# Performance work log

Measured on AMD Instinct MI355X. Metric: run time of the kernel, lower is better.

The kernel has to match this reference:

```python
import jax, jax.numpy as jnp
import numpy as np

H, T, D = 16, 2048, 1024
DH = D // H  # 64


def setup_inputs() -> dict:
    key = jax.random.key(0)
    ks = jax.random.split(key, 6)
    state = jax.random.normal(ks[0], (H, DH, DH), jnp.float32) * 0.02  # per-head recurrent state
    x = jax.random.normal(ks[1], (T, D), jnp.float32)
    done = jax.random.uniform(ks[2], (T,)) < (4.0 / T)  # sparse episode-reset flags (bool)
    w_qkv = jax.random.normal(ks[3], (D, 3 * D), jnp.float32) / np.sqrt(D)
    b_qkv = jnp.zeros((3 * D,), jnp.float32)
    w_out = jax.random.normal(ks[4], (D, D), jnp.float32) / np.sqrt(D)
    b_out = jnp.zeros((D,), jnp.float32)
    return {"state": state, "x": x, "done": done, "w_qkv": w_qkv,
            "b_qkv": b_qkv, "w_out": w_out, "b_out": b_out}


def _mha_forward(state, x, done, w_qkv, b_qkv, w_out, b_out):
    # qkv projection; einops 'T (QKV H Dh) -> QKV H T Dh'
    qkv = (x @ w_qkv + b_qkv).reshape(T, 3, H, DH).transpose(1, 2, 0, 3)
    q, k, v = qkv[0], qkv[1], qkv[2]  # each (H, T, Dh)

    cum = jnp.cumsum(done.astype(jnp.int32))  # inclusive cumsum, as in done.cumsum()
    before_first = cum == 0            # tokens before first reset (attend to carried state)
    after_last = cum == cum[-1]        # tokens after last reset (feed new state)
    done_any = cum[-1] > 0

    # make_attn_mask(done): causal AND no reset index i with s < i <= t.
    # The scanned mask equals: causal & (cum[t] == cum[s]) (same-segment).
    t_idx = jnp.arange(T)
    mask = (t_idx[:, None] >= t_idx[None, :]) & (cum[:, None] == cum[None, :])  # (T, T)

    attn = jnp.where(mask[None], jnp.einsum('htd,hsd->hts', q, k), 0.0)  # mask * (q @ k.T)
    q_bef = q * before_first[None, :, None]
    out = jnp.einsum('hts,hsd->htd', attn, v) + jnp.einsum('htd,hde->hte', q_bef, state)

    k_aft = k * after_last[None, :, None]
    v_aft = v * after_last[None, :, None]
    s_new = jnp.einsum('htd,hte->hde', k_aft, v_aft)  # k_aft.T @ v_aft per head
    new_state = jnp.where(done_any, s_new, state + s_new)

    # 'H T Dh -> T (H Dh)' then output projection
    x_out = out.transpose(1, 0, 2).reshape(T, D) @ w_out + b_out
    return new_state, x_out


def reference(state, x, done, w_qkv, b_qkv, w_out, b_out):
    return _mha_forward(state, x, done, w_qkv, b_qkv, w_out, b_out)
```

## Files before the change

kernel.cpp:

```cpp
#include <hip/hip_runtime.h>

#define TT 2048
#define DD 1024
#define HH 16
#define DH 64
#define QKV_N 3072
#define QKW 2048

typedef __attribute__((ext_vector_type(8))) short bf16x8;
typedef __attribute__((ext_vector_type(4))) short short4v;
typedef __attribute__((ext_vector_type(4))) float f32x4;

__device__ inline short f2bf(float f) {
    union { float f; unsigned u; } v; v.f = f;
    unsigned r = v.u + 0x7fff + ((v.u >> 16) & 1);
    return (short)(r >> 16);
}

__device__ inline f32x4 mfma16(bf16x8 a, bf16x8 b, f32x4 c) {
    return __builtin_amdgcn_mfma_f32_16x16x32_bf16(a, b, c, 0, 0, 0);
}

__device__ __forceinline__ void gload16(const void* g, void* l) {
    __builtin_amdgcn_global_load_lds(
        (const __attribute__((address_space(1))) unsigned int*)g,
        (__attribute__((address_space(3))) unsigned int*)l, 16, 0, 0);
}

__device__ void transpose_tile(const float* __restrict__ in, short* __restrict__ out,
                               int R, int C, int r0, int c0, float (*tile)[65]) {
    int tid = threadIdx.x;
#pragma unroll
    for (int p = 0; p < 4; ++p) {
        int ch = tid + p * 256;
        int r = ch >> 4, c4 = (ch & 15) * 4;
        float4 v = *(const float4*)&in[(size_t)(r0 + r) * C + c0 + c4];
        tile[r][c4] = v.x; tile[r][c4 + 1] = v.y; tile[r][c4 + 2] = v.z; tile[r][c4 + 3] = v.w;
    }
    __syncthreads();
#pragma unroll
    for (int p = 0; p < 2; ++p) {
        int ch = tid + p * 256;
        int c = ch >> 3, r8 = (ch & 7) * 8;
        short tmp[8];
#pragma unroll
        for (int i = 0; i < 8; ++i) tmp[i] = f2bf(tile[r8 + i][c]);
        *(float4*)&out[(size_t)(c0 + c) * R + r0 + r8] = *(float4*)tmp;
    }
}

__global__ __launch_bounds__(256) void prep_kernel(const float* __restrict__ x,
                                                   const float* __restrict__ w_qkv,
                                                   const float* __restrict__ w_out,
                                                   const float* __restrict__ state,
                                                   const int* __restrict__ done,
                                                   short* __restrict__ x_bf,
                                                   short* __restrict__ wqT,
                                                   short* __restrict__ woT,
                                                   short* __restrict__ stT,
                                                   float* __restrict__ stout,
                                                   int* __restrict__ seg,
                                                   int* __restrict__ totalp,
                                                   int* __restrict__ aux) {
    __shared__ float tile[64][65];
    __shared__ int scanbuf[2048 + 512 + 1];
    int b = blockIdx.x;
    int tid = threadIdx.x;
    if (b < 1024) {
        int i = (b * 256 + tid) * 8;
        float4 a = *(const float4*)&x[i];
        float4 c = *(const float4*)&x[i + 4];
        short tmp[8] = {f2bf(a.x), f2bf(a.y), f2bf(a.z), f2bf(a.w),
                        f2bf(c.x), f2bf(c.y), f2bf(c.z), f2bf(c.w)};
        *(float4*)&x_bf[i] = *(float4*)tmp;
    } else if (b < 1792) {
        int bb = b - 1024;
        transpose_tile(w_qkv, wqT, DD, QKV_N, (bb & 15) * 64, (bb >> 4) * 64, tile);
    } else if (b < 2048) {
        int bb = b - 1792;
        transpose_tile(w_out, woT, DD, DD, (bb & 15) * 64, (bb >> 4) * 64, tile);
    } else if (b < 2064) {
        int h = b - 2048;
        transpose_tile(state + (size_t)h * 4096, stT + (size_t)h * 4096, DH, DH, 0, 0, tile);
    } else if (b < 2128) {
        __shared__ int anyf;
        if (tid == 0) anyf = 0;
        __syncthreads();
        int acc = 0;
#pragma unroll
        for (int i = 0; i < 8; ++i) acc |= done[tid * 8 + i];
        if (acc) anyf = 1;
        __syncthreads();
        int f = ((b - 2064) * 256 + tid) * 4;
        float4 v = anyf ? make_float4(0.f, 0.f, 0.f, 0.f) : *(const float4*)&state[f];
        *(float4*)&stout[f] = v;
    } else {
        int* segl = scanbuf;
        int* part = scanbuf + 2048;
        int* excl = scanbuf + 2304;
        int base = tid * 8;
        int local[8];
        int run = 0;
#pragma unroll
        for (int i = 0; i < 8; ++i) { run += (done[base + i] != 0) ? 1 : 0; local[i] = run; }
        part[tid] = run;
        __syncthreads();
        if (tid < 64) {
            int p4[4];
#pragma unroll
            for (int i = 0; i < 4; ++i) p4[i] = part[tid * 4 + i];
            int s = p4[0] + p4[1] + p4[2] + p4[3];
            int v = s;
#pragma unroll
            for (int off = 1; off < 64; off <<= 1) {
                int u = __shfl_up(v, off);
                if (tid >= off) v += u;
            }
            int ex = v - s;
#pragma unroll
            for (int i = 0; i < 4; ++i) { excl[tid * 4 + i] = ex; ex += p4[i]; }
            if (tid == 63) { totalp[0] = v; scanbuf[2560] = v; }
        }
        __syncthreads();
        int off = excl[tid];
#pragma unroll
        for (int i = 0; i < 8; ++i) {
            int sv = off + local[i];
            seg[base + i] = sv;
            segl[base + i] = sv;
        }
        __syncthreads();
        if (tid < 33) {
            int target = (tid < 32) ? segl[tid * 64] : scanbuf[2560];
            int lo = 0, hi = 2047;
            while (lo < hi) { int mid = (lo + hi) >> 1; if (segl[mid] >= target) hi = mid; else lo = mid + 1; }
            aux[tid] = lo >> 6;
        }
    }
}

__global__ __launch_bounds__(256, 3) void gemm_qkv(const short* __restrict__ A,
                                                   const short* __restrict__ BT,
                                                   const float* __restrict__ bias,
                                                   short* __restrict__ qk,
                                                   short* __restrict__ vt) {
    __shared__ __align__(16) short As[2][2][64 * 32];
    __shared__ __align__(16) short Bs[2][2][128 * 32];
    const int K = DD;
    int tid = threadIdx.x;
    int wave = tid >> 6, lane = tid & 63;
    int quad = lane >> 4, l15 = lane & 15;
    int m0 = blockIdx.x * 64, n0 = blockIdx.y * 128;
    int wr = (wave >> 1) * 32, wc = (wave & 1) * 64;

    int srow = wave * 16 + (lane >> 2);
    int scol = (lane & 3) * 8;
    const short* Ag = A + (size_t)(m0 + srow) * K + scol;
    const short* Bg = BT + (size_t)(n0 + srow) * K + scol;

#pragma unroll
    for (int ks = 0; ks < 2; ++ks) {
        gload16(Ag + ks * 32, &As[0][ks][(wave * 16) * 32]);
        gload16(Bg + ks * 32, &Bs[0][ks][(wave * 16) * 32]);
        gload16(Bg + (size_t)64 * K + ks * 32, &Bs[0][ks][(64 + wave * 16) * 32]);
    }
    __syncthreads();

    f32x4 acc[2][4] = {};
    int cur = 0;
    for (int k0 = 0; k0 < K; k0 += 64, cur ^= 1) {
        if (k0 + 64 < K) {
#pragma unroll
            for (int ks = 0; ks < 2; ++ks) {
                gload16(Ag + k0 + 64 + ks * 32, &As[cur ^ 1][ks][(wave * 16) * 32]);
                gload16(Bg + k0 + 64 + ks * 32, &Bs[cur ^ 1][ks][(wave * 16) * 32]);
                gload16(Bg + (size_t)64 * K + k0 + 64 + ks * 32,
                        &Bs[cur ^ 1][ks][(64 + wave * 16) * 32]);
            }
        }
#pragma unroll
        for (int ks = 0; ks < 2; ++ks) {
            bf16x8 af[2], bfr[4];
#pragma unroll
            for (int i = 0; i < 2; ++i)
                af[i]  = *(const bf16x8*)&As[cur][ks][(wr + i * 16 + l15) * 32 + quad * 8];
#pragma unroll
            for (int j = 0; j < 4; ++j)
                bfr[j] = *(const bf16x8*)&Bs[cur][ks][(wc + j * 16 + l15) * 32 + quad * 8];
#pragma unroll
            for (int i = 0; i < 2; ++i)
#pragma unroll
                for (int j = 0; j < 4; ++j)
                    acc[i][j] = mfma16(af[i], bfr[j], acc[i][j]);
        }
        __syncthreads();
    }

    if (n0 < 2048) {
#pragma unroll
        for (int i = 0; i < 2; ++i)
#pragma unroll
            for (int j = 0; j < 4; ++j)
#pragma unroll
                for (int r = 0; r < 4; ++r) {
                    int row = m0 + wr + i * 16 + quad * 4 + r;
                    int col = n0 + wc + j * 16 + l15;
                    qk[(size_t)row * QKW + col] = f2bf(acc[i][j][r] + bias[col]);
                }
    } else {
#pragma unroll
        for (int j = 0; j < 4; ++j) {
            int col = n0 + wc + j * 16 + l15;
            float bv = bias[col];
            int eg = col - 2048;
            int hh = eg >> 6, e = eg & 63;
#pragma unroll
            for (int i = 0; i < 2; ++i) {
                int tb = m0 + wr + i * 16 + quad * 4;
                short4v pk;
#pragma unroll
                for (int r = 0; r < 4; ++r) pk[r] = f2bf(acc[i][j][r] + bv);
                *(short4v*)&vt[(size_t)hh * (DH * TT) + (size_t)e * TT + tb] = pk;
            }
        }
    }
}

__global__ __launch_bounds__(256) void attn_mfma(const short* __restrict__ qk,
                                                 const short* __restrict__ vt,
                                                 const short* __restrict__ stT,
                                                 const int* __restrict__ seg,
                                                 const int* __restrict__ totalp,
                                                 const int* __restrict__ aux,
                                                 short* __restrict__ outb,
                                                 float* __restrict__ nsout) {
    __shared__ __align__(16) short Qh[2][64 * 32];
    __shared__ __align__(16) short Kh[2][2][64 * 32];
    __shared__ __align__(16) short Vh[2][2][64 * 32];
    __shared__ __align__(16) short Ss[64 * 72];

    int h = blockIdx.x, tt = blockIdx.y, z = blockIdx.z;
    int t0 = tt * 64;
    int tid = threadIdx.x, wave = tid >> 6, lane = tid & 63;
    int quad = lane >> 4, l15 = lane & 15;
    int myt = wave * 16;
    const short* vbase = vt + (size_t)h * (DH * TT);

    if (z == 1) {
        if (tt < aux[32]) return;
        int total = totalp[0];
        int myd = wave * 16;
        short* K0 = Kh[0][0];
        short* K1 = Kh[0][1];
        bool keep = (seg[t0 + lane] == total);
        const short* src = qk + (size_t)(t0 + lane) * QKW + 1024 + h * DH + myd;
        union { float4 f; short s[8]; } u0, u1;
        u0.f = keep ? *(const float4*)src : make_float4(0.f, 0.f, 0.f, 0.f);
        u1.f = keep ? *(const float4*)(src + 8) : make_float4(0.f, 0.f, 0.f, 0.f);
        short* dst = (lane < 32) ? &K0[lane] : &K1[lane - 32];
#pragma unroll
        for (int i = 0; i < 8; ++i) {
            dst[(myd + i) * 32] = u0.s[i];
            dst[(myd + 8 + i) * 32] = u1.s[i];
        }
        bf16x8 a0 = *(const bf16x8*)&K0[(myd + l15) * 32 + quad * 8];
        bf16x8 a1 = *(const bf16x8*)&K1[(myd + l15) * 32 + quad * 8];
        f32x4 acc2[4] = {};
#pragma unroll
        for (int j = 0; j < 4; ++j) {
            const short* vrow = vbase + (size_t)(j * 16 + l15) * TT + t0 + quad * 8;
            bf16x8 b0 = *(const bf16x8*)vrow;
            bf16x8 b1 = *(const bf16x8*)(vrow + 32);
            acc2[j] = mfma16(a0, b0, acc2[j]);
            acc2[j] = mfma16(a1, b1, acc2[j]);
        }
        float* oh = nsout + (size_t)h * 4096;
#pragma unroll
        for (int j = 0; j < 4; ++j)
#pragma unroll
            for (int r = 0; r < 4; ++r)
                atomicAdd(&oh[(myd + quad * 4 + r) * DH + j * 16 + l15], acc2[j][r]);
        return;
    }

    int st0 = aux[tt];
    int sr = lane >> 2;
    int ch = lane & 3;
    const short* kg = qk + 1024 + h * DH;

    {
#pragma unroll
        for (int h2 = 0; h2 < 2; ++h2)
            gload16(qk + (size_t)(t0 + myt + sr) * QKW + h * DH + h2 * 32 + ch * 8,
                    &Qh[h2][myt * 32]);
        int s0 = st0 * 64;
        gload16(kg + (size_t)(s0 + myt + sr) * QKW + ch * 8,      &Kh[0][0][myt * 32]);
        gload16(kg + (size_t)(s0 + myt + sr) * QKW + 32 + ch * 8, &Kh[0][1][myt * 32]);
        gload16(vbase + (size_t)(myt + sr) * TT + s0 + ch * 8,    &Vh[0][0][myt * 32]);
        gload16(vbase + (size_t)(myt + sr) * TT + s0 + 32 + ch * 8, &Vh[0][1][myt * 32]);
    }
    __syncthreads();

    bf16x8 af[2];
#pragma unroll
    for (int h2 = 0; h2 < 2; ++h2)
        af[h2] = *(const bf16x8*)&Qh[h2][(myt + l15) * 32 + quad * 8];

    int t_val = t0 + myt + l15;
    int seg_lane = seg[t_val];

    f32x4 acc2[4] = {};
    if (seg[t0] == 0) {
        const short* sb = stT + (size_t)h * 4096;
#pragma unroll
        for (int j = 0; j < 4; ++j)
#pragma unroll
            for (int h2 = 0; h2 < 2; ++h2) {
                bf16x8 a = *(const bf16x8*)(sb + (j * 16 + l15) * 64 + h2 * 32 + quad * 8);
                acc2[j] = mfma16(a, af[h2], acc2[j]);
            }
        if (seg_lane != 0) {
#pragma unroll
            for (int j = 0; j < 4; ++j)
#pragma unroll
                for (int r = 0; r < 4; ++r) acc2[j][r] = 0.f;
        }
    }

    int p = 0;
    for (int st = st0; st <= tt; ++st, p ^= 1) {
        if (st != st0) __syncthreads();
        if (st + 1 <= tt) {
            int s1 = (st + 1) * 64;
            gload16(kg + (size_t)(s1 + myt + sr) * QKW + ch * 8,        &Kh[p ^ 1][0][myt * 32]);
            gload16(kg + (size_t)(s1 + myt + sr) * QKW + 32 + ch * 8,   &Kh[p ^ 1][1][myt * 32]);
            gload16(vbase + (size_t)(myt + sr) * TT + s1 + ch * 8,      &Vh[p ^ 1][0][myt * 32]);
            gload16(vbase + (size_t)(myt + sr) * TT + s1 + 32 + ch * 8, &Vh[p ^ 1][1][myt * 32]);
        }
        int s0 = st * 64;

        f32x4 sacc[4] = {};
#pragma unroll
        for (int j = 0; j < 4; ++j)
#pragma unroll
            for (int h2 = 0; h2 < 2; ++h2) {
                bf16x8 kb = *(const bf16x8*)&Kh[p][h2][(j * 16 + l15) * 32 + quad * 8];
                sacc[j] = mfma16(kb, af[h2], sacc[j]);
            }
        int4 seg4[4];
#pragma unroll
        for (int j = 0; j < 4; ++j)
            seg4[j] = *(const int4*)&seg[s0 + j * 16 + quad * 4];
#pragma unroll
        for (int j = 0; j < 4; ++j) {
            short4v pk;
#pragma unroll
            for (int r = 0; r < 4; ++r) {
                int s_val = s0 + j * 16 + quad * 4 + r;
                int sv = (r == 0) ? seg4[j].x : (r == 1) ? seg4[j].y : (r == 2) ? seg4[j].z : seg4[j].w;
                bool ok = (sv == seg_lane) && (s_val <= t_val);
                pk[r] = ok ? f2bf(sacc[j][r]) : (short)0;
            }
            *(short4v*)&Ss[(myt + l15) * 72 + j * 16 + quad * 4] = pk;
        }
        bf16x8 sf[2];
#pragma unroll
        for (int h2 = 0; h2 < 2; ++h2)
            sf[h2] = *(const bf16x8*)&Ss[(myt + l15) * 72 + h2 * 32 + quad * 8];
#pragma unroll
        for (int j = 0; j < 4; ++j)
#pragma unroll
            for (int h2 = 0; h2 < 2; ++h2) {
                bf16x8 vb = *(const bf16x8*)&Vh[p][h2][(j * 16 + l15) * 32 + quad * 8];
                acc2[j] = mfma16(vb, sf[h2], acc2[j]);
            }
    }

#pragma unroll
    for (int j = 0; j < 4; ++j) {
        short4v pk;
#pragma unroll
        for (int r = 0; r < 4; ++r) pk[r] = f2bf(acc2[j][r]);
        *(short4v*)&outb[(size_t)t_val * DD + h * DH + j * 16 + quad * 4] = pk;
    }
}

__global__ __launch_bounds__(256) void gemm_out(const short* __restrict__ A,
                                                const short* __restrict__ BT,
                                                const float* __restrict__ bias,
                                                float* __restrict__ x_out) {
    __shared__ __align__(16) short As[2][2][64 * 32];
    __shared__ __align__(16) short Bs[2][2][128 * 32];
    const int K = DD, N = DD;
    int tid = threadIdx.x;
    int wave = tid >> 6, lane = tid & 63;
    int quad = lane >> 4, l15 = lane & 15;
    int m0 = blockIdx.x * 64, n0 = blockIdx.y * 128;
    int wr = (wave >> 1) * 32, wc = (wave & 1) * 64;

    int srow = wave * 16 + (lane >> 2);
    int scol = (lane & 3) * 8;
    const short* Ag = A + (size_t)(m0 + srow) * K + scol;
    const short* Bg = BT + (size_t)(n0 + srow) * K + scol;

#pragma unroll
    for (int ks = 0; ks < 2; ++ks) {
        gload16(Ag + ks * 32, &As[0][ks][(wave * 16) * 32]);
        gload16(Bg + ks * 32, &Bs[0][ks][(wave * 16) * 32]);
        gload16(Bg + (size_t)64 * K + ks * 32, &Bs[0][ks][(64 + wave * 16) * 32]);
    }
    __syncthreads();

    f32x4 acc[2][4] = {};
    int cur = 0;
    for (int k0 = 0; k0 < K; k0 += 64, cur ^= 1) {
        if (k0 + 64 < K) {
#pragma unroll
            for (int ks = 0; ks < 2; ++ks) {
                gload16(Ag + k0 + 64 + ks * 32, &As[cur ^ 1][ks][(wave * 16) * 32]);
                gload16(Bg + k0 + 64 + ks * 32, &Bs[cur ^ 1][ks][(wave * 16) * 32]);
                gload16(Bg + (size_t)64 * K + k0 + 64 + ks * 32,
                        &Bs[cur ^ 1][ks][(64 + wave * 16) * 32]);
            }
        }
#pragma unroll
        for (int ks = 0; ks < 2; ++ks) {
            bf16x8 af[2], bfr[4];
#pragma unroll
            for (int i = 0; i < 2; ++i)
                af[i]  = *(const bf16x8*)&As[cur][ks][(wr + i * 16 + l15) * 32 + quad * 8];
#pragma unroll
            for (int j = 0; j < 4; ++j)
                bfr[j] = *(const bf16x8*)&Bs[cur][ks][(wc + j * 16 + l15) * 32 + quad * 8];
#pragma unroll
            for (int i = 0; i < 2; ++i)
#pragma unroll
                for (int j = 0; j < 4; ++j)
                    acc[i][j] = mfma16(af[i], bfr[j], acc[i][j]);
        }
        __syncthreads();
    }

#pragma unroll
    for (int i = 0; i < 2; ++i)
#pragma unroll
        for (int j = 0; j < 4; ++j) {
            int col = n0 + wc + j * 16 + l15;
            float bv = bias[col];
#pragma unroll
            for (int r = 0; r < 4; ++r) {
                int row = m0 + wr + i * 16 + quad * 4 + r;
                x_out[(size_t)row * N + col] = acc[i][j][r] + bv;
            }
        }
}

extern "C" void kernel_launch(void* const* d_in, const int* in_sizes, int n_in,
                              void* d_out, int out_size, void* d_ws, size_t ws_size,
                              hipStream_t stream) {
    const float* state = (const float*)d_in[0];
    const float* x     = (const float*)d_in[1];
    const int*   done  = (const int*)d_in[2];
    const float* w_qkv = (const float*)d_in[3];
    const float* b_qkv = (const float*)d_in[4];
    const float* w_out = (const float*)d_in[5];
    const float* b_out = (const float*)d_in[6];

    char* ws = (char*)d_ws;
    int*   seg    = (int*)ws;
    int*   totalp = (int*)(ws + 8192);
    int*   aux    = (int*)(ws + 8256);
    short* wqT    = (short*)(ws + 8448);
    short* woT    = (short*)(ws + 6299904);
    short* stT    = (short*)(ws + 8397056);
    short* qk     = (short*)(ws + 8528128);
    short* vt     = (short*)(ws + 16916736);
    short* xbf_outb = (short*)(ws + 21111040);

    float* new_state_out = (float*)d_out;
    float* x_out         = (float*)d_out + HH * DH * DH;

    prep_kernel<<<2129, 256, 0, stream>>>(x, w_qkv, w_out, state, done,
                                          xbf_outb, wqT, woT, stT,
                                          new_state_out, seg, totalp, aux);

    gemm_qkv<<<dim3(TT / 64, QKV_N / 128), 256, 0, stream>>>(
        xbf_outb, wqT, b_qkv, qk, vt);

    attn_mfma<<<dim3(HH, TT / 64, 2), 256, 0, stream>>>(
        qk, vt, stT, seg, totalp, aux, xbf_outb, new_state_out);

    gemm_out<<<dim3(TT / 64, DD / 128), 256, 0, stream>>>(
        xbf_outb, woT, b_out, x_out);
}
```

Measured before the change: 147.2 us.

## Fuse four kernels into one persistent kernel with software grid barriers

The prep, QKV GEMM, attention and output GEMM kernels are merged into one persistent kernel of 512 blocks. Each block loops over the virtual block indices of each phase, and the phases are separated by an atomic grid barrier. Shared memory is overlaid with a union. The goal is to remove the launch gaps and tail effects between kernels. The cost is barrier spinning, a bound of 2 blocks per CU that can limit occupancy, a deadlock risk if not all 512 blocks are resident (there is a timeout break), and an extra memset.

```diff
diff --git a/kernel.cpp b/kernel.cpp
--- a/kernel.cpp
+++ b/kernel.cpp
@@ -6,6 +6,7 @@
 #define DH 64
 #define QKV_N 3072
 #define QKW 2048
+#define NBLK 512
 
 typedef __attribute__((ext_vector_type(8))) short bf16x8;
 typedef __attribute__((ext_vector_type(4))) short short4v;
@@ -26,6 +27,31 @@
         (const __attribute__((address_space(1))) unsigned int*)g,
         (__attribute__((address_space(3))) unsigned int*)l, 16, 0, 0);
 }
+
+__device__ __forceinline__ void gbar(int* cnt, int* flag, int target) {
+    __syncthreads();
+    if (threadIdx.x == 0) {
+        int t = __hip_atomic_fetch_add(cnt, 1, __ATOMIC_ACQ_REL, __HIP_MEMORY_SCOPE_AGENT);
+        if (t == NBLK - 1) {
+            __hip_atomic_store(cnt, 0, __ATOMIC_RELAXED, __HIP_MEMORY_SCOPE_AGENT);
+            __hip_atomic_fetch_add(flag, 1, __ATOMIC_RELEASE, __HIP_MEMORY_SCOPE_AGENT);
+        } else {
+            long long t0 = clock64();
+            while (__hip_atomic_load(flag, __ATOMIC_ACQUIRE, __HIP_MEMORY_SCOPE_AGENT) < target) {
+                if (clock64() - t0 > 60000000LL) break;
+                __builtin_amdgcn_s_sleep(2);
+            }
+        }
+    }
+    __syncthreads();
+}
+
+union SharedMem {
+    struct { short As[2][2][64 * 32]; short Bs[2][2][128 * 32]; } g;
+    struct { short Qh[2][64 * 32]; short Kh[2][2][64 * 32];
+             short Vh[2][2][64 * 32]; short Ss[64 * 72]; } a;
+    struct { float tile[64][65]; int scanbuf[2561]; } p;
+};
 
 __device__ void transpose_tile(const float* __restrict__ in, short* __restrict__ out,
                                int R, int C, int r0, int c0, float (*tile)[65]) {
@@ -49,417 +75,399 @@
     }
 }
 
-__global__ __launch_bounds__(256) void prep_kernel(const float* __restrict__ x,
-                                                   const float* __restrict__ w_qkv,
-                                                   const float* __restrict__ w_out,
-                                                   const float* __restrict__ state,
-                                                   const int* __restrict__ done,
-                                                   short* __restrict__ x_bf,
-                                                   short* __restrict__ wqT,
-                                                   short* __restrict__ woT,
-                                                   short* __restrict__ stT,
-                                                   float* __restrict__ stout,
-                                                   int* __restrict__ seg,
-                                                   int* __restrict__ totalp,
-                                                   int* __restrict__ aux) {
-    __shared__ float tile[64][65];
-    __shared__ int scanbuf[2048 + 512 + 1];
-    int b = blockIdx.x;
-    int tid = threadIdx.x;
-    if (b < 1024) {
-        int i = (b * 256 + tid) * 8;
-        float4 a = *(const float4*)&x[i];
-        float4 c = *(const float4*)&x[i + 4];
-        short tmp[8] = {f2bf(a.x), f2bf(a.y), f2bf(a.z), f2bf(a.w),
-                        f2bf(c.x), f2bf(c.y), f2bf(c.z), f2bf(c.w)};
-        *(float4*)&x_bf[i] = *(float4*)tmp;
-    } else if (b < 1792) {
-        int bb = b - 1024;
-        transpose_tile(w_qkv, wqT, DD, QKV_N, (bb & 15) * 64, (bb >> 4) * 64, tile);
-    } else if (b < 2048) {
-        int bb = b - 1792;
-        transpose_tile(w_out, woT, DD, DD, (bb & 15) * 64, (bb >> 4) * 64, tile);
-    } else if (b < 2064) {
-        int h = b - 2048;
-        transpose_tile(state + (size_t)h * 4096, stT + (size_t)h * 4096, DH, DH, 0, 0, tile);
-    } else if (b < 2128) {
-        __shared__ int anyf;
-        if (tid == 0) anyf = 0;
-        __syncthreads();
-        int acc = 0;
-#pragma unroll
-        for (int i = 0; i < 8; ++i) acc |= done[tid * 8 + i];
-        if (acc) anyf = 1;
-        __syncthreads();
-        int f = ((b - 2064) * 256 + tid) * 4;
-        float4 v = anyf ? make_float4(0.f, 0.f, 0.f, 0.f) : *(const float4*)&state[f];
-        *(float4*)&stout[f] = v;
-    } else {
-        int* segl = scanbuf;
-        int* part = scanbuf + 2048;
-        int* excl = scanbuf + 2304;
-        int base = tid * 8;
-        int local[8];
-        int run = 0;
-#pragma unroll
-        for (int i = 0; i < 8; ++i) { run += (done[base + i] != 0) ? 1 : 0; local[i] = run; }
-        part[tid] = run;
-        __syncthreads();
-        if (tid < 64) {
-            int p4[4];
-#pragma unroll
-            for (int i = 0; i < 4; ++i) p4[i] = part[tid * 4 + i];
-            int s = p4[0] + p4[1] + p4[2] + p4[3];
-            int v = s;
-#pragma unroll
-            for (int off = 1; off < 64; off <<= 1) {
-                int u = __shfl_up(v, off);
-                if (tid >= off) v += u;
-            }
-            int ex = v - s;
-#pragma unroll
-            for (int i = 0; i < 4; ++i) { excl[tid * 4 + i] = ex; ex += p4[i]; }
-            if (tid == 63) { totalp[0] = v; scanbuf[2560] = v; }
-        }
-        __syncthreads();
-        int off = excl[tid];
-#pragma unroll
-        for (int i = 0; i < 8; ++i) {
-            int sv = off + local[i];
-            seg[base + i] = sv;
-            segl[base + i] = sv;
-        }
-        __syncthreads();
-        if (tid < 33) {
-            int target = (tid < 32) ? segl[tid * 64] : scanbuf[2560];
-            int lo = 0, hi = 2047;
-            while (lo < hi) { int mid = (lo + hi) >> 1; if (segl[mid] >= target) hi = mid; else lo = mid + 1; }
-            aux[tid] = lo >> 6;
-        }
-    }
-}
-
-__global__ __launch_bounds__(256, 3) void gemm_qkv(const short* __restrict__ A,
-                                                   const short* __restrict__ BT,
-                                                   const float* __restrict__ bias,
-                                                   short* __restrict__ qk,
-                                                   short* __restrict__ vt) {
-    __shared__ __align__(16) short As[2][2][64 * 32];
-    __shared__ __align__(16) short Bs[2][2][128 * 32];
-    const int K = DD;
+__global__ __launch_bounds__(256, 2) void fused_kernel(
+    const float* __restrict__ x, const float* __restrict__ w_qkv,
+    const float* __restrict__ w_out, const float* __restrict__ state,
+    const int* __restrict__ done, const float* __restrict__ b_qkv,
+    const float* __restrict__ b_out,
+    short* __restrict__ xo,
+    short* __restrict__ wqT, short* __restrict__ woT, short* __restrict__ stT,
+    short* __restrict__ qk, short* __restrict__ vt,
+    float* __restrict__ nsout, float* __restrict__ x_out,
+    int* __restrict__ seg, int* __restrict__ totalp, int* __restrict__ aux,
+    int* __restrict__ bar) {
+    __shared__ __align__(16) SharedMem sh;
+    __shared__ int anyf;
+    int* cnt = bar;
+    int* flag = bar + 4;
+
+    int bid = blockIdx.x;
     int tid = threadIdx.x;
     int wave = tid >> 6, lane = tid & 63;
     int quad = lane >> 4, l15 = lane & 15;
-    int m0 = blockIdx.x * 64, n0 = blockIdx.y * 128;
-    int wr = (wave >> 1) * 32, wc = (wave & 1) * 64;
-
-    int srow = wave * 16 + (lane >> 2);
-    int scol = (lane & 3) * 8;
-    const short* Ag = A + (size_t)(m0 + srow) * K + scol;
-    const short* Bg = BT + (size_t)(n0 + srow) * K + scol;
-
-#pragma unroll
-    for (int ks = 0; ks < 2; ++ks) {
-        gload16(Ag + ks * 32, &As[0][ks][(wave * 16) * 32]);
-        gload16(Bg + ks * 32, &Bs[0][ks][(wave * 16) * 32]);
-        gload16(Bg + (size_t)64 * K + ks * 32, &Bs[0][ks][(64 + wave * 16) * 32]);
-    }
-    __syncthreads();
-
-    f32x4 acc[2][4] = {};
-    int cur = 0;
-    for (int k0 = 0; k0 < K; k0 += 64, cur ^= 1) {
-        if (k0 + 64 < K) {
+
+    for (int vb = bid; vb < 2129; vb += NBLK) {
+        __syncthreads();
+        int b = vb;
+        if (b < 1024) {
+            int i = (b * 256 + tid) * 8;
+            float4 a = *(const float4*)&x[i];
+            float4 c = *(const float4*)&x[i + 4];
+            short tmp[8] = {f2bf(a.x), f2bf(a.y), f2bf(a.z), f2bf(a.w),
+                            f2bf(c.x), f2bf(c.y), f2bf(c.z), f2bf(c.w)};
+            *(float4*)&xo[i] = *(float4*)tmp;
+        } else if (b < 1792) {
+            int bb = b - 1024;
+            transpose_tile(w_qkv, wqT, DD, QKV_N, (bb & 15) * 64, (bb >> 4) * 64, sh.p.tile);
+        } else if (b < 2048) {
+            int bb = b - 1792;
+            transpose_tile(w_out, woT, DD, DD, (bb & 15) * 64, (bb >> 4) * 64, sh.p.tile);
+        } else if (b < 2064) {
+            int h = b - 2048;
+            transpose_tile(state + (size_t)h * 4096, stT + (size_t)h * 4096, DH, DH, 0, 0, sh.p.tile);
+        } else if (b < 2128) {
+            if (tid == 0) anyf = 0;
+            __syncthreads();
+            int acc = 0;
+#pragma unroll
+            for (int i = 0; i < 8; ++i) acc |= done[tid * 8 + i];
+            if (acc) anyf = 1;
+            __syncthreads();
+            int f = ((b - 2064) * 256 + tid) * 4;
+            float4 v = anyf ? make_float4(0.f, 0.f, 0.f, 0.f) : *(const float4*)&state[f];
+            *(float4*)&nsout[f] = v;
+        } else {
+            int* segl = sh.p.scanbuf;
+            int* part = sh.p.scanbuf + 2048;
+            int* excl = sh.p.scanbuf + 2304;
+            int base = tid * 8;
+            int local[8];
+            int run = 0;
+#pragma unroll
+            for (int i = 0; i < 8; ++i) { run += (done[base + i] != 0) ? 1 : 0; local[i] = run; }
+            part[tid] = run;
+            __syncthreads();
+            if (tid < 64) {
+                int p4[4];
+#pragma unroll
+                for (int i = 0; i < 4; ++i) p4[i] = part[tid * 4 + i];
+                int s = p4[0] + p4[1] + p4[2] + p4[3];
+                int v = s;
+#pragma unroll
+                for (int off = 1; off < 64; off <<= 1) {
+                    int u = __shfl_up(v, off);
+                    if (tid >= off) v += u;
+                }
+                int ex = v - s;
+#pragma unroll
+                for (int i = 0; i < 4; ++i) { excl[tid * 4 + i] = ex; ex += p4[i]; }
+                if (tid == 63) { totalp[0] = v; sh.p.scanbuf[2560] = v; }
+            }
+            __syncthreads();
+            int off = excl[tid];
+#pragma unroll
+            for (int i = 0; i < 8; ++i) {
+                int sv = off + local[i];
+                seg[base + i] = sv;
+                segl[base + i] = sv;
+            }
+            __syncthreads();
+            if (tid < 33) {
+                int target = (tid < 32) ? segl[tid * 64] : sh.p.scanbuf[2560];
+                int lo = 0, hi = 2047;
+                while (lo < hi) { int mid = (lo + hi) >> 1; if (segl[mid] >= target) hi = mid; else lo = mid + 1; }
+                aux[tid] = lo >> 6;
+            }
+        }
+    }
+    gbar(cnt, flag, 1);
+
+    for (int vb = bid; vb < 768; vb += NBLK) {
+        __syncthreads();
+        const int K = DD;
+        int m0 = (vb & 31) * 64, n0 = (vb >> 5) * 128;
+        int wr = (wave >> 1) * 32, wc = (wave & 1) * 64;
+        int srow = wave * 16 + (lane >> 2);
+        int scol = (lane & 3) * 8;
+        const short* Ag = xo + (size_t)(m0 + srow) * K + scol;
+        const short* Bg = wqT + (size_t)(n0 + srow) * K + scol;
+
+#pragma unroll
+        for (int ks = 0; ks < 2; ++ks) {
+            gload16(Ag + ks * 32, &sh.g.As[0][ks][(wave * 16) * 32]);
+            gload16(Bg + ks * 32, &sh.g.Bs[0][ks][(wave * 16) * 32]);
+            gload16(Bg + (size_t)64 * K + ks * 32, &sh.g.Bs[0][ks][(64 + wave * 16) * 32]);
+        }
+        __syncthreads();
+
+        f32x4 acc[2][4] = {};
+        int cur = 0;
+        for (int k0 = 0; k0 < K; k0 += 64, cur ^= 1) {
+            if (k0 + 64 < K) {
+#pragma unroll
+                for (int ks = 0; ks < 2; ++ks) {
+                    gload16(Ag + k0 + 64 + ks * 32, &sh.g.As[cur ^ 1][ks][(wave * 16) * 32]);
+                    gload16(Bg + k0 + 64 + ks * 32, &sh.g.Bs[cur ^ 1][ks][(wave * 16) * 32]);
+                    gload16(Bg + (size_t)64 * K + k0 + 64 + ks * 32,
+                            &sh.g.Bs[cur ^ 1][ks][(64 + wave * 16) * 32]);
+                }
+            }
 #pragma unroll
             for (int ks = 0; ks < 2; ++ks) {
-                gload16(Ag + k0 + 64 + ks * 32, &As[cur ^ 1][ks][(wave * 16) * 32]);
-                gload16(Bg + k0 + 64 + ks * 32, &Bs[cur ^ 1][ks][(wave * 16) * 32]);
-                gload16(Bg + (size_t)64 * K + k0 + 64 + ks * 32,
-                        &Bs[cur ^ 1][ks][(64 + wave * 16) * 32]);
-            }
-        }
+                bf16x8 af[2], bfr[4];
+#pragma unroll
+                for (int i = 0; i < 2; ++i)
+                    af[i]  = *(const bf16x8*)&sh.g.As[cur][ks][(wr + i * 16 + l15) * 32 + quad * 8];
+#pragma unroll
+                for (int j = 0; j < 4; ++j)
+                    bfr[j] = *(const bf16x8*)&sh.g.Bs[cur][ks][(wc + j * 16 + l15) * 32 + quad * 8];
+#pragma unroll
+                for (int i = 0; i < 2; ++i)
+#pragma unroll
+                    for (int j = 0; j < 4; ++j)
+                        acc[i][j] = mfma16(af[i], bfr[j], acc[i][j]);
+            }
+            __syncthreads();
+        }
+
+        if (n0 < 2048) {
+#pragma unroll
+            for (int i = 0; i < 2; ++i)
+#pragma unroll
+                for (int j = 0; j < 4; ++j)
+#pragma unroll
+                    for (int r = 0; r < 4; ++r) {
+                        int row = m0 + wr + i * 16 + quad * 4 + r;
+                        int col = n0 + wc + j * 16 + l15;
+                        qk[(size_t)row * QKW + col] = f2bf(acc[i][j][r] + b_qkv[col]);
+                    }
+        } else {
+#pragma unroll
+            for (int j = 0; j < 4; ++j) {
+                int col = n0 + wc + j * 16 + l15;
+                float bv = b_qkv[col];
+                int eg = col - 2048;
+                int hh = eg >> 6, e = eg & 63;
+#pragma unroll
+                for (int i = 0; i < 2; ++i) {
+                    int tb = m0 + wr + i * 16 + quad * 4;
+                    short4v pk;
+#pragma unroll
+                    for (int r = 0; r < 4; ++r) pk[r] = f2bf(acc[i][j][r] + bv);
+                    *(short4v*)&vt[(size_t)hh * (DH * TT) + (size_t)e * TT + tb] = pk;
+                }
+            }
+        }
+    }
+    gbar(cnt, flag, 2);
+
+    for (int vb = bid; vb < 1024; vb += NBLK) {
+        __syncthreads();
+        int z = vb >> 9;
+        int rem = vb & 511;
+        int h = rem & 15, tt = rem >> 4;
+        int t0 = tt * 64;
+        int myt = wave * 16;
+        const short* vbase = vt + (size_t)h * (DH * TT);
+
+        if (z == 1) {
+            if (tt >= aux[32]) {
+                int total = totalp[0];
+                int myd = wave * 16;
+                short* K0 = sh.a.Kh[0][0];
+                short* K1 = sh.a.Kh[0][1];
+                bool keep = (seg[t0 + lane] == total);
+                const short* src = qk + (size_t)(t0 + lane) * QKW + 1024 + h * DH + myd;
+                union { float4 f; short s[8]; } u0, u1;
+                u0.f = keep ? *(const float4*)src : make_float4(0.f, 0.f, 0.f, 0.f);
+                u1.f = keep ? *(const float4*)(src + 8) : make_float4(0.f, 0.f, 0.f, 0.f);
+                short* dst = (lane < 32) ? &K0[lane] : &K1[lane - 32];
+#pragma unroll
+                for (int i = 0; i < 8; ++i) {
+                    dst[(myd + i) * 32] = u0.s[i];
+                    dst[(myd + 8 + i) * 32] = u1.s[i];
+                }
+                bf16x8 a0 = *(const bf16x8*)&K0[(myd + l15) * 32 + quad * 8];
+                bf16x8 a1 = *(const bf16x8*)&K1[(myd + l15) * 32 + quad * 8];
+                f32x4 acc2[4] = {};
+#pragma unroll
+                for (int j = 0; j < 4; ++j) {
+                    const short* vrow = vbase + (size_t)(j * 16 + l15) * TT + t0 + quad * 8;
+                    bf16x8 b0 = *(const bf16x8*)vrow;
+                    bf16x8 b1 = *(const bf16x8*)(vrow + 32);
+                    acc2[j] = mfma16(a0, b0, acc2[j]);
+                    acc2[j] = mfma16(a1, b1, acc2[j]);
+                }
+                float* oh = nsout + (size_t)h * 4096;
+#pragma unroll
+                for (int j = 0; j < 4; ++j)
+#pragma unroll
+                    for (int r = 0; r < 4; ++r)
+                        atomicAdd(&oh[(myd + quad * 4 + r) * DH + j * 16 + l15], acc2[j][r]);
+            }
+            continue;
+        }
+
+        int st0 = aux[tt];
+        int sr = lane >> 2;
+        int ch = lane & 3;
+        const short* kg = qk + 1024 + h * DH;
+
+        {
+#pragma unroll
+            for (int h2 = 0; h2 < 2; ++h2)
+                gload16(qk + (size_t)(t0 + myt + sr) * QKW + h * DH + h2 * 32 + ch * 8,
+                        &sh.a.Qh[h2][myt * 32]);
+            int s0 = st0 * 64;
+            gload16(kg + (size_t)(s0 + myt + sr) * QKW + ch * 8,        &sh.a.Kh[0][0][myt * 32]);
+            gload16(kg + (size_t)(s0 + myt + sr) * QKW + 32 + ch * 8,   &sh.a.Kh[0][1][myt * 32]);
+            gload16(vbase + (size_t)(myt + sr) * TT + s0 + ch * 8,      &sh.a.Vh[0][0][myt * 32]);
+            gload16(vbase + (size_t)(myt + sr) * TT + s0 + 32 + ch * 8, &sh.a.Vh[0][1][myt * 32]);
+        }
+        __syncthreads();
+
+        bf16x8 af[2];
+#pragma unroll
+        for (int h2 = 0; h2 < 2; ++h2)
+            af[h2] = *(const bf16x8*)&sh.a.Qh[h2][(myt + l15) * 32 + quad * 8];
+
+        int t_val = t0 + myt + l15;
+        int seg_lane = seg[t_val];
+
+        f32x4 acc2[4] = {};
+        if (seg[t0] == 0) {
+            const short* sb = stT + (size_t)h * 4096;
+#pragma unroll
+            for (int j = 0; j < 4; ++j)
+#pragma unroll
+                for (int h2 = 0; h2 < 2; ++h2) {
+                    bf16x8 a = *(const bf16x8*)(sb + (j * 16 + l15) * 64 + h2 * 32 + quad * 8);
+                    acc2[j] = mfma16(a, af[h2], acc2[j]);
+                }
+            if (seg_lane != 0) {
+#pragma unroll
+                for (int j = 0; j < 4; ++j)
+#pragma unroll
+                    for (int r = 0; r < 4; ++r) acc2[j][r] = 0.f;
+            }
+        }
+
+        int p = 0;
+        for (int st = st0; st <= tt; ++st, p ^= 1) {
+            if (st != st0) __syncthreads();
+            if (st + 1 <= tt) {
+                int s1 = (st + 1) * 64;
+                gload16(kg + (size_t)(s1 + myt + sr) * QKW + ch * 8,        &sh.a.Kh[p ^ 1][0][myt * 32]);
+                gload16(kg + (size_t)(s1 + myt + sr) * QKW + 32 + ch * 8,   &sh.a.Kh[p ^ 1][1][myt * 32]);
+                gload16(vbase + (size_t)(myt + sr) * TT + s1 + ch * 8,      &sh.a.Vh[p ^ 1][0][myt * 32]);
+                gload16(vbase + (size_t)(myt + sr) * TT + s1 + 32 + ch * 8, &sh.a.Vh[p ^ 1][1][myt * 32]);
+            }
+            int s0 = st * 64;
+
+            f32x4 sacc[4] = {};
+#pragma unroll
+            for (int j = 0; j < 4; ++j)
+#pragma unroll
+                for (int h2 = 0; h2 < 2; ++h2) {
+                    bf16x8 kb = *(const bf16x8*)&sh.a.Kh[p][h2][(j * 16 + l15) * 32 + quad * 8];
+                    sacc[j] = mfma16(kb, af[h2], sacc[j]);
+                }
+            int4 seg4[4];
+#pragma unroll
+            for (int j = 0; j < 4; ++j)
+                seg4[j] = *(const int4*)&seg[s0 + j * 16 + quad * 4];
+#pragma unroll
+            for (int j = 0; j < 4; ++j) {
+                short4v pk;
+#pragma unroll
+                for (int r = 0; r < 4; ++r) {
+                    int s_val = s0 + j * 16 + quad * 4 + r;
+                    int sv = (r == 0) ? seg4[j].x : (r == 1) ? seg4[j].y : (r == 2) ? seg4[j].z : seg4[j].w;
+                    bool ok = (sv == seg_lane) && (s_val <= t_val);
+                    pk[r] = ok ? f2bf(sacc[j][r]) : (short)0;
+                }
+                *(short4v*)&sh.a.Ss[(myt + l15) * 72 + j * 16 + quad * 4] = pk;
+            }
+            bf16x8 sf[2];
+#pragma unroll
+            for (int h2 = 0; h2 < 2; ++h2)
+                sf[h2] = *(const bf16x8*)&sh.a.Ss[(myt + l15) * 72 + h2 * 32 + quad * 8];
+#pragma unroll
+            for (int j = 0; j < 4; ++j)
+#pragma unroll
+                for (int h2 = 0; h2 < 2; ++h2) {
+                    bf16x8 vb2 = *(const bf16x8*)&sh.a.Vh[p][h2][(j * 16 + l15) * 32 + quad * 8];
+                    acc2[j] = mfma16(vb2, sf[h2], acc2[j]);
+                }
+        }
+
+#pragma unroll
+        for (int j = 0; j < 4; ++j) {
+            short4v pk;
+#pragma unroll
+            for (int r = 0; r < 4; ++r) pk[r] = f2bf(acc2[j][r]);
+            *(short4v*)&xo[(size_t)t_val * DD + h * DH + j * 16 + quad * 4] = pk;
+        }
+    }
+    gbar(cnt, flag, 3);
+
+    if (bid < 256) {
+        const int K = DD, N = DD;
+        int m0 = (bid & 31) * 64, n0 = (bid >> 5) * 128;
+        int wr = (wave >> 1) * 32, wc = (wave & 1) * 64;
+        int srow = wave * 16 + (lane >> 2);
+        int scol = (lane & 3) * 8;
+        const short* Ag = xo + (size_t)(m0 + srow) * K + scol;
+        const short* Bg = woT + (size_t)(n0 + srow) * K + scol;
+
 #pragma unroll
         for (int ks = 0; ks < 2; ++ks) {
-            bf16x8 af[2], bfr[4];
-#pragma unroll
-            for (int i = 0; i < 2; ++i)
-                af[i]  = *(const bf16x8*)&As[cur][ks][(wr + i * 16 + l15) * 32 + quad * 8];
-#pragma unroll
-            for (int j = 0; j < 4; ++j)
-                bfr[j] = *(const bf16x8*)&Bs[cur][ks][(wc + j * 16 + l15) * 32 + quad * 8];
-#pragma unroll
-            for (int i = 0; i < 2; ++i)
+            gload16(Ag + ks * 32, &sh.g.As[0][ks][(wave * 16) * 32]);
+            gload16(Bg + ks * 32, &sh.g.Bs[0][ks][(wave * 16) * 32]);
+            gload16(Bg + (size_t)64 * K + ks * 32, &sh.g.Bs[0][ks][(64 + wave * 16) * 32]);
+        }
+        __syncthreads();
+
+        f32x4 acc[2][4] = {};
+        int cur = 0;
+        for (int k0 = 0; k0 < K; k0 += 64, cur ^= 1) {
+            if (k0 + 64 < K) {
+#pragma unroll
+                for (int ks = 0; ks < 2; ++ks) {
+                    gload16(Ag + k0 + 64 + ks * 32, &sh.g.As[cur ^ 1][ks][(wave * 16) * 32]);
+                    gload16(Bg + k0 + 64 + ks * 32, &sh.g.Bs[cur ^ 1][ks][(wave * 16) * 32]);
+                    gload16(Bg + (size_t)64 * K + k0 + 64 + ks * 32,
+                            &sh.g.Bs[cur ^ 1][ks][(64 + wave * 16) * 32]);
+                }
+            }
+#pragma unroll
+            for (int ks = 0; ks < 2; ++ks) {
+                bf16x8 af2[2], bfr[4];
+#pragma unroll
+                for (int i = 0; i < 2; ++i)
+                    af2[i] = *(const bf16x8*)&sh.g.As[cur][ks][(wr + i * 16 + l15) * 32 + quad * 8];
 #pragma unroll
                 for (int j = 0; j < 4; ++j)
-                    acc[i][j] = mfma16(af[i], bfr[j], acc[i][j]);
-        }
-        __syncthreads();
-    }
-
-    if (n0 < 2048) {
+                    bfr[j] = *(const bf16x8*)&sh.g.Bs[cur][ks][(wc + j * 16 + l15) * 32 + quad * 8];
+#pragma unroll
+                for (int i = 0; i < 2; ++i)
+#pragma unroll
+                    for (int j = 0; j < 4; ++j)
+                        acc[i][j] = mfma16(af2[i], bfr[j], acc[i][j]);
+            }
+            __syncthreads();
+        }
+
 #pragma unroll
         for (int i = 0; i < 2; ++i)
 #pragma unroll
-            for (int j = 0; j < 4; ++j)
+            for (int j = 0; j < 4; ++j) {
+                int col = n0 + wc + j * 16 + l15;
+                float bv = b_out[col];
 #pragma unroll
                 for (int r = 0; r < 4; ++r) {
                     int row = m0 + wr + i * 16 + quad * 4 + r;
-                    int col = n0 + wc + j * 16 + l15;
-                    qk[(size_t)row * QKW + col] = f2bf(acc[i][j][r] + bias[col]);
-                }
-    } else {
-#pragma unroll
-        for (int j = 0; j < 4; ++j) {
-            int col = n0 + wc + j * 16 + l15;
-            float bv = bias[col];
-            int eg = col - 2048;
-            int hh = eg >> 6, e = eg & 63;
-#pragma unroll
-            for (int i = 0; i < 2; ++i) {
-                int tb = m0 + wr + i * 16 + quad * 4;
-                short4v pk;
-#pragma unroll
-                for (int r = 0; r < 4; ++r) pk[r] = f2bf(acc[i][j][r] + bv);
-                *(short4v*)&vt[(size_t)hh * (DH * TT) + (size_t)e * TT + tb] = pk;
-            }
-        }
-    }
-}
-
-__global__ __launch_bounds__(256) void attn_mfma(const short* __restrict__ qk,
-                                                 const short* __restrict__ vt,
-                                                 const short* __restrict__ stT,
-                                                 const int* __restrict__ seg,
-                                                 const int* __restrict__ totalp,
-                                                 const int* __restrict__ aux,
-                                                 short* __restrict__ outb,
-                                                 float* __restrict__ nsout) {
-    __shared__ __align__(16) short Qh[2][64 * 32];
-    __shared__ __align__(16) short Kh[2][2][64 * 32];
-    __shared__ __align__(16) short Vh[2][2][64 * 32];
-    __shared__ __align__(16) short Ss[64 * 72];
-
-    int h = blockIdx.x, tt = blockIdx.y, z = blockIdx.z;
-    int t0 = tt * 64;
-    int tid = threadIdx.x, wave = tid >> 6, lane = tid & 63;
-    int quad = lane >> 4, l15 = lane & 15;
-    int myt = wave * 16;
-    const short* vbase = vt + (size_t)h * (DH * TT);
-
-    if (z == 1) {
-        if (tt < aux[32]) return;
-        int total = totalp[0];
-        int myd = wave * 16;
-        short* K0 = Kh[0][0];
-        short* K1 = Kh[0][1];
-        bool keep = (seg[t0 + lane] == total);
-        const short* src = qk + (size_t)(t0 + lane) * QKW + 1024 + h * DH + myd;
-        union { float4 f; short s[8]; } u0, u1;
-        u0.f = keep ? *(const float4*)src : make_float4(0.f, 0.f, 0.f, 0.f);
-        u1.f = keep ? *(const float4*)(src + 8) : make_float4(0.f, 0.f, 0.f, 0.f);
-        short* dst = (lane < 32) ? &K0[lane] : &K1[lane - 32];
-#pragma unroll
-        for (int i = 0; i < 8; ++i) {
-            dst[(myd + i) * 32] = u0.s[i];
-            dst[(myd + 8 + i) * 32] = u1.s[i];
-        }
-        bf16x8 a0 = *(const bf16x8*)&K0[(myd + l15) * 32 + quad * 8];
-        bf16x8 a1 = *(const bf16x8*)&K1[(myd + l15) * 32 + quad * 8];
-        f32x4 acc2[4] = {};
-#pragma unroll
-        for (int j = 0; j < 4; ++j) {
-            const short* vrow = vbase + (size_t)(j * 16 + l15) * TT + t0 + quad * 8;
-            bf16x8 b0 = *(const bf16x8*)vrow;
-            bf16x8 b1 = *(const bf16x8*)(vrow + 32);
-            acc2[j] = mfma16(a0, b0, acc2[j]);
-            acc2[j] = mfma16(a1, b1, acc2[j]);
-        }
-        float* oh = nsout + (size_t)h * 4096;
-#pragma unroll
-        for (int j = 0; j < 4; ++j)
-#pragma unroll
-            for (int r = 0; r < 4; ++r)
-                atomicAdd(&oh[(myd + quad * 4 + r) * DH + j * 16 + l15], acc2[j][r]);
-        return;
-    }
-
-    int st0 = aux[tt];
-    int sr = lane >> 2;
-    int ch = lane & 3;
-    const short* kg = qk + 1024 + h * DH;
-
-    {
-#pragma unroll
-        for (int h2 = 0; h2 < 2; ++h2)
-            gload16(qk + (size_t)(t0 + myt + sr) * QKW + h * DH + h2 * 32 + ch * 8,
-                    &Qh[h2][myt * 32]);
-        int s0 = st0 * 64;
-        gload16(kg + (size_t)(s0 + myt + sr) * QKW + ch * 8,      &Kh[0][0][myt * 32]);
-        gload16(kg + (size_t)(s0 + myt + sr) * QKW + 32 + ch * 8, &Kh[0][1][myt * 32]);
-        gload16(vbase + (size_t)(myt + sr) * TT + s0 + ch * 8,    &Vh[0][0][myt * 32]);
-        gload16(vbase + (size_t)(myt + sr) * TT + s0 + 32 + ch * 8, &Vh[0][1][myt * 32]);
-    }
-    __syncthreads();
-
-    bf16x8 af[2];
-#pragma unroll
-    for (int h2 = 0; h2 < 2; ++h2)
-        af[h2] = *(const bf16x8*)&Qh[h2][(myt + l15) * 32 + quad * 8];
-
-    int t_val = t0 + myt + l15;
-    int seg_lane = seg[t_val];
-
-    f32x4 acc2[4] = {};
-    if (seg[t0] == 0) {
-        const short* sb = stT + (size_t)h * 4096;
-#pragma unroll
-        for (int j = 0; j < 4; ++j)
-#pragma unroll
-            for (int h2 = 0; h2 < 2; ++h2) {
-                bf16x8 a = *(const bf16x8*)(sb + (j * 16 + l15) * 64 + h2 * 32 + quad * 8);
-                acc2[j] = mfma16(a, af[h2], acc2[j]);
-            }
-        if (seg_lane != 0) {
-#pragma unroll
-            for (int j = 0; j < 4; ++j)
-#pragma unroll
-                for (int r = 0; r < 4; ++r) acc2[j][r] = 0.f;
-        }
-    }
-
-    int p = 0;
-    for (int st = st0; st <= tt; ++st, p ^= 1) {
-        if (st != st0) __syncthreads();
-        if (st + 1 <= tt) {
-            int s1 = (st + 1) * 64;
-            gload16(kg + (size_t)(s1 + myt + sr) * QKW + ch * 8,        &Kh[p ^ 1][0][myt * 32]);
-            gload16(kg + (size_t)(s1 + myt + sr) * QKW + 32 + ch * 8,   &Kh[p ^ 1][1][myt * 32]);
-            gload16(vbase + (size_t)(myt + sr) * TT + s1 + ch * 8,      &Vh[p ^ 1][0][myt * 32]);
-            gload16(vbase + (size_t)(myt + sr) * TT + s1 + 32 + ch * 8, &Vh[p ^ 1][1][myt * 32]);
-        }
-        int s0 = st * 64;
-
-        f32x4 sacc[4] = {};
-#pragma unroll
-        for (int j = 0; j < 4; ++j)
-#pragma unroll
-            for (int h2 = 0; h2 < 2; ++h2) {
-                bf16x8 kb = *(const bf16x8*)&Kh[p][h2][(j * 16 + l15) * 32 + quad * 8];
-                sacc[j] = mfma16(kb, af[h2], sacc[j]);
-            }
-        int4 seg4[4];
-#pragma unroll
-        for (int j = 0; j < 4; ++j)
-            seg4[j] = *(const int4*)&seg[s0 + j * 16 + quad * 4];
-#pragma unroll
-        for (int j = 0; j < 4; ++j) {
-            short4v pk;
-#pragma unroll
-            for (int r = 0; r < 4; ++r) {
-                int s_val = s0 + j * 16 + quad * 4 + r;
-                int sv = (r == 0) ? seg4[j].x : (r == 1) ? seg4[j].y : (r == 2) ? seg4[j].z : seg4[j].w;
-                bool ok = (sv == seg_lane) && (s_val <= t_val);
-                pk[r] = ok ? f2bf(sacc[j][r]) : (short)0;
-            }
-            *(short4v*)&Ss[(myt + l15) * 72 + j * 16 + quad * 4] = pk;
-        }
-        bf16x8 sf[2];
-#pragma unroll
-        for (int h2 = 0; h2 < 2; ++h2)
-            sf[h2] = *(const bf16x8*)&Ss[(myt + l15) * 72 + h2 * 32 + quad * 8];
-#pragma unroll
-        for (int j = 0; j < 4; ++j)
-#pragma unroll
-            for (int h2 = 0; h2 < 2; ++h2) {
-                bf16x8 vb = *(const bf16x8*)&Vh[p][h2][(j * 16 + l15) * 32 + quad * 8];
-                acc2[j] = mfma16(vb, sf[h2], acc2[j]);
-            }
-    }
-
-#pragma unroll
-    for (int j = 0; j < 4; ++j) {
-        short4v pk;
-#pragma unroll
-        for (int r = 0; r < 4; ++r) pk[r] = f2bf(acc2[j][r]);
-        *(short4v*)&outb[(size_t)t_val * DD + h * DH + j * 16 + quad * 4] = pk;
-    }
-}
-
-__global__ __launch_bounds__(256) void gemm_out(const short* __restrict__ A,
-                                                const short* __restrict__ BT,
-                                                const float* __restrict__ bias,
-                                                float* __restrict__ x_out) {
-    __shared__ __align__(16) short As[2][2][64 * 32];
-    __shared__ __align__(16) short Bs[2][2][128 * 32];
-    const int K = DD, N = DD;
-    int tid = threadIdx.x;
-    int wave = tid >> 6, lane = tid & 63;
-    int quad = lane >> 4, l15 = lane & 15;
-    int m0 = blockIdx.x * 64, n0 = blockIdx.y * 128;
-    int wr = (wave >> 1) * 32, wc = (wave & 1) * 64;
-
-    int srow = wave * 16 + (lane >> 2);
-    int scol = (lane & 3) * 8;
-    const short* Ag = A + (size_t)(m0 + srow) * K + scol;
-    const short* Bg = BT + (size_t)(n0 + srow) * K + scol;
-
-#pragma unroll
-    for (int ks = 0; ks < 2; ++ks) {
-        gload16(Ag + ks * 32, &As[0][ks][(wave * 16) * 32]);
-        gload16(Bg + ks * 32, &Bs[0][ks][(wave * 16) * 32]);
-        gload16(Bg + (size_t)64 * K + ks * 32, &Bs[0][ks][(64 + wave * 16) * 32]);
-    }
-    __syncthreads();
-
-    f32x4 acc[2][4] = {};
-    int cur = 0;
-    for (int k0 = 0; k0 < K; k0 += 64, cur ^= 1) {
-        if (k0 + 64 < K) {
-#pragma unroll
-            for (int ks = 0; ks < 2; ++ks) {
-                gload16(Ag + k0 + 64 + ks * 32, &As[cur ^ 1][ks][(wave * 16) * 32]);
-                gload16(Bg + k0 + 64 + ks * 32, &Bs[cur ^ 1][ks][(wave * 16) * 32]);
-                gload16(Bg + (size_t)64 * K + k0 + 64 + ks * 32,
-                        &Bs[cur ^ 1][ks][(64 + wave * 16) * 32]);
-            }
-        }
-#pragma unroll
-        for (int ks = 0; ks < 2; ++ks) {
-            bf16x8 af[2], bfr[4];
-#pragma unroll
-            for (int i = 0; i < 2; ++i)
-                af[i]  = *(const bf16x8*)&As[cur][ks][(wr + i * 16 + l15) * 32 + quad * 8];
-#pragma unroll
-            for (int j = 0; j < 4; ++j)
-                bfr[j] = *(const bf16x8*)&Bs[cur][ks][(wc + j * 16 + l15) * 32 + quad * 8];
-#pragma unroll
-            for (int i = 0; i < 2; ++i)
-#pragma unroll
-                for (int j = 0; j < 4; ++j)
-                    acc[i][j] = mfma16(af[i], bfr[j], acc[i][j]);
-        }
-        __syncthreads();
-    }
-
-#pragma unroll
-    for (int i = 0; i < 2; ++i)
-#pragma unroll
-        for (int j = 0; j < 4; ++j) {
-            int col = n0 + wc + j * 16 + l15;
-            float bv = bias[col];
-#pragma unroll
-            for (int r = 0; r < 4; ++r) {
-                int row = m0 + wr + i * 16 + quad * 4 + r;
-                x_out[(size_t)row * N + col] = acc[i][j][r] + bv;
-            }
-        }
+                    x_out[(size_t)row * N + col] = acc[i][j][r] + bv;
+                }
+            }
+    }
 }
 
 extern "C" void kernel_launch(void* const* d_in, const int* in_sizes, int n_in,
                               void* d_out, int out_size, void* d_ws, size_t ws_size,
                               hipStream_t stream) {
     const float* state = (const float*)d_in[0];
-    const float* x     = (const float*)d_in[1];
+    const float* x_in  = (const float*)d_in[1];
     const int*   done  = (const int*)d_in[2];
     const float* w_qkv = (const float*)d_in[3];
     const float* b_qkv = (const float*)d_in[4];
@@ -470,26 +478,21 @@
     int*   seg    = (int*)ws;
     int*   totalp = (int*)(ws + 8192);
     int*   aux    = (int*)(ws + 8256);
+    int*   bar    = (int*)(ws + 8400);
     short* wqT    = (short*)(ws + 8448);
     short* woT    = (short*)(ws + 6299904);
     short* stT    = (short*)(ws + 8397056);
     short* qk     = (short*)(ws + 8528128);
     short* vt     = (short*)(ws + 16916736);
-    short* xbf_outb = (short*)(ws + 21111040);
-
-    float* new_state_out = (float*)d_out;
-    float* x_out         = (float*)d_out + HH * DH * DH;
-
-    prep_kernel<<<2129, 256, 0, stream>>>(x, w_qkv, w_out, state, done,
-                                          xbf_outb, wqT, woT, stT,
-                                          new_state_out, seg, totalp, aux);
-
-    gemm_qkv<<<dim3(TT / 64, QKV_N / 128), 256, 0, stream>>>(
-        xbf_outb, wqT, b_qkv, qk, vt);
-
-    attn_mfma<<<dim3(HH, TT / 64, 2), 256, 0, stream>>>(
-        qk, vt, stT, seg, totalp, aux, xbf_outb, new_state_out);
-
-    gemm_out<<<dim3(TT / 64, DD / 128), 256, 0, stream>>>(
-        xbf_outb, woT, b_out, x_out);
-}
+    short* xo     = (short*)(ws + 21111040);
+
+    float* nsout = (float*)d_out;
+    float* x_out = (float*)d_out + HH * DH * DH;
+
+    hipMemsetAsync(bar, 0, 32, stream);
+
+    fused_kernel<<<NBLK, 256, 0, stream>>>(
+        x_in, w_qkv, w_out, state, done, b_qkv, b_out,
+        xo, wqT, woT, stT, qk, vt, nsout, x_out,
+        seg, totalp, aux, bar);
+}
```

After: 442.7 us. 201% more time.
